# Kernel tuning notes

Hardware: AMD Instinct MI355X
Metric: run time of the kernel (lower is better)

Reference implementation:

```python
import jax, jax.numpy as jnp
import numpy as np

LOG_SCALE_INIT = float(np.log(10.0))


def lorentz_linear(x, W, b, log_scale):
    # nonlin (gelu) -> linear -> Lorentz time/space renormalization
    y = jax.nn.gelu(x) @ W.T + b
    time = jax.nn.sigmoid(y[..., :1]) * jnp.exp(log_scale) + 1.1
    nar = y[..., 1:]
    denom = jnp.clip(jnp.sum(nar * nar, axis=-1, keepdims=True), 1e-8, None)
    scale = (time * time - 1.0) / denom
    return jnp.concatenate([time, nar * jnp.sqrt(scale)], axis=-1)


def ffn_lorentz(x, W1, b1, s1, W2, b2, s2):
    return lorentz_linear(lorentz_linear(x, W1, b1, s1), W2, b2, s2) + x


def knn_indices(x, k):
    # x: (B,N,C). KNN on detached features (as in ViG dense_knn_matrix).
    xs = jax.lax.stop_gradient(x)
    sq = jnp.sum(xs * xs, axis=-1)  # (B,N)
    d = sq[:, :, None] + sq[:, None, :] - 2.0 * jnp.einsum('bnc,bmc->bnm', xs, xs)
    _, idx = jax.lax.top_k(-d, k)  # (B,N,k) nearest (includes self)
    return idx


def graph_conv(x, Wg, bg, sg, k):
    # Max-relative graph conv with Lorentz linear. x: (B,N,C)
    idx = knn_indices(x, k)
    xj = jax.vmap(lambda xb, ib: xb[ib])(x, idx)  # (B,N,k,C) gather
    msg = jnp.max(xj - x[:, :, None, :], axis=2)  # (B,N,C)
    h = jnp.concatenate([x, msg], axis=-1)        # (B,N,2C)
    return lorentz_linear(h, Wg, bg, sg)


def setup_inputs() -> dict:
    key = jax.random.key(0)
    ks = jax.random.split(key, 8)
    B, C, H, W = 8, 192, 56, 56
    x = jax.random.normal(ks[0], (B, C, H, W), dtype=jnp.float32)
    def lin(k_, fin, fout):
        return jax.random.normal(k_, (fout, fin), dtype=jnp.float32) * 0.02
    p = {
        'x': x,
        'W1': lin(ks[1], C, C), 'b1': jnp.zeros((C,), jnp.float32), 's1': jnp.float32(LOG_SCALE_INIT),
        'W2': lin(ks[2], C, C), 'b2': jnp.zeros((C,), jnp.float32), 's2': jnp.float32(LOG_SCALE_INIT),
        'Wg': lin(ks[3], 2 * C, C), 'bg': jnp.zeros((C,), jnp.float32), 'sg': jnp.float32(LOG_SCALE_INIT),
        'W3': lin(ks[4], C, C), 'b3': jnp.zeros((C,), jnp.float32), 's3': jnp.float32(LOG_SCALE_INIT),
        'W4': lin(ks[5], C, C), 'b4': jnp.zeros((C,), jnp.float32), 's4': jnp.float32(LOG_SCALE_INIT),
        'k': 9,
    }
    return p


def reference(x, W1, b1, s1, W2, b2, s2, Wg, bg, sg, W3, b3, s3, W4, b4, s4, k):
    B, C, H, W = x.shape
    xn = x.reshape(B, C, H * W).transpose(0, 2, 1)  # (B,N,C) == rearrange b c (h w) 1 -> b (h w) c
    shortcut = xn
    xn = ffn_lorentz(xn, W1, b1, s1, W2, b2, s2)
    xn = graph_conv(xn, Wg, bg, sg, k)
    xn = ffn_lorentz(xn, W3, b3, s3, W4, b4, s4)
    xn = xn + shortcut  # drop_path = 0 -> identity
    return xn.transpose(0, 2, 1).reshape(B, C, H, W)
```

## Files before the change

kernel.cpp:

```cpp
#include <hip/hip_runtime.h>
#include <math.h>

#define NB   8
#define NC   192
#define NPIX 3136
#define NPAD 3200
#define GRID_LL (NB*98)
#define NIT  25
#define NSP  8
#define GRID_KNN (NB*NIT*NSP)
#define GRID_MSG (NB*196)
#define FINF 3.4e38f

typedef _Float16 f16x8 __attribute__((ext_vector_type(8)));
typedef float   f32x16 __attribute__((ext_vector_type(16)));

__device__ __forceinline__ float gelu_f(float x){
    float u = 0.7978845608028654f * (x + 0.044715f * x * x * x);
    return 0.5f * x * (1.0f + tanhf(u));
}

#define LESS9(da,ia,db,ib) ((da) < (db) || ((da) == (db) && (ia) < (ib)))
#define CSW9(a,ia,b,ib) { bool sw_ = LESS9(b,ib,a,ia); float tf_=(a); int ti_=(ia); \
    (a) = sw_? (b) : (a); (ia) = sw_? (ib) : (ia); (b) = sw_? tf_ : (b); (ib) = sw_? ti_ : (ib); }

struct Top9 {
    float d0,d1,d2,d3,d4,d5,d6,d7,d8;
    int   j0,j1,j2,j3,j4,j5,j6,j7,j8;
    __device__ __forceinline__ void init(){
        d0=d1=d2=d3=d4=d5=d6=d7=d8=FINF;
        j0=j1=j2=j3=j4=j5=j6=j7=j8=0x7FFFFFFF;
    }
    __device__ __forceinline__ void insert(float nd, int ni){
        if (!LESS9(nd, ni, d8, j8)) return;
        d8 = nd; j8 = ni;
        CSW9(d7,j7,d8,j8); CSW9(d6,j6,d7,j7); CSW9(d5,j5,d6,j6); CSW9(d4,j4,d5,j5);
        CSW9(d3,j3,d4,j4); CSW9(d2,j2,d3,j3); CSW9(d1,j1,d2,j2); CSW9(d0,j0,d1,j1);
    }
};

__device__ __forceinline__ unsigned f2mono(float e){
    unsigned u = __float_as_uint(e);
    return u ^ ((unsigned)((int)u >> 31) | 0x80000000u);
}

#define CSK(a,b) { unsigned h_ = (a) > (b) ? (a) : (b); unsigned l_ = (a) > (b) ? (b) : (a); (a) = h_; (b) = l_; }
#define INSKEY(x_) if ((x_) > t_k11){ t_k11 = (x_); \
    CSK(t_k10,t_k11) CSK(t_k9,t_k10) CSK(t_k8,t_k9) CSK(t_k7,t_k8) \
    CSK(t_k6,t_k7) CSK(t_k5,t_k6) CSK(t_k4,t_k5) CSK(t_k3,t_k4) \
    CSK(t_k2,t_k3) CSK(t_k1,t_k2) CSK(t_k0,t_k1) }

#define KQ(A,Q) { \
    unsigned q0_ = (f2mono(A[4*(Q)+0]) & 0xFFFFF000u) | (unsigned)(jinvb_ - 8*(Q)    ); \
    unsigned q1_ = (f2mono(A[4*(Q)+1]) & 0xFFFFF000u) | (unsigned)(jinvb_ - 8*(Q) - 1); \
    unsigned q2_ = (f2mono(A[4*(Q)+2]) & 0xFFFFF000u) | (unsigned)(jinvb_ - 8*(Q) - 2); \
    unsigned q3_ = (f2mono(A[4*(Q)+3]) & 0xFFFFF000u) | (unsigned)(jinvb_ - 8*(Q) - 3); \
    unsigned qa_ = q0_ > q1_ ? q0_ : q1_; \
    unsigned qb_ = q2_ > q3_ ? q2_ : q3_; \
    unsigned qm_ = qa_ > qb_ ? qa_ : qb_; \
    if (qm_ > t_k11){ INSKEY(q0_) INSKEY(q1_) INSKEY(q2_) INSKEY(q3_) } }

#define INSACCK(A,JS) { int jinvb_ = 4095 - (jg + (JS)*32 + 4*h); \
    KQ(A,0) KQ(A,1) KQ(A,2) KQ(A,3) }

#define MF(ACC,AO,BO) ACC = __builtin_amdgcn_mfma_f32_32x32x16_f16(AO,BO,ACC,0,0,0);
#define ZERO16 {0,0,0,0,0,0,0,0,0,0,0,0,0,0,0,0}

__global__ __launch_bounds__(256) void wt_kernel(
    const float* __restrict__ W1, const float* __restrict__ W2,
    const float* __restrict__ Wg, const float* __restrict__ W3,
    const float* __restrict__ W4,
    float* __restrict__ W1T, float* __restrict__ W2T, float* __restrict__ WgT,
    float* __restrict__ W3T, float* __restrict__ W4T)
{
    __shared__ float tile[32*33];
    int t = blockIdx.x;
    const float* src; float* dst; int Kin;
    if (t < 36)      { src = W1; dst = W1T; Kin = 192; }
    else if (t < 72) { src = W2; dst = W2T; Kin = 192; t -= 36; }
    else if (t < 144){ src = Wg; dst = WgT; Kin = 384; t -= 72; }
    else if (t < 180){ src = W3; dst = W3T; Kin = 192; t -= 144; }
    else             { src = W4; dst = W4T; Kin = 192; t -= 180; }
    int ntc = Kin >> 5;
    int tr = t / ntc, tc = t - tr*ntc;
    int tid = threadIdx.x;
    {
        int i = tid >> 3, j4 = (tid & 7)*4;
        float4 v = *(const float4*)&src[(size_t)(tr*32 + i)*Kin + tc*32 + j4];
        tile[i*33 + j4+0] = v.x; tile[i*33 + j4+1] = v.y;
        tile[i*33 + j4+2] = v.z; tile[i*33 + j4+3] = v.w;
    }
    __syncthreads();
    {
        int j = tid >> 3, i4 = (tid & 7)*4;
        float4 o = make_float4(tile[(i4+0)*33 + j], tile[(i4+1)*33 + j],
                               tile[(i4+2)*33 + j], tile[(i4+3)*33 + j]);
        *(float4*)&dst[(size_t)(tc*32 + j)*192 + tr*32 + i4] = o;
    }
}

template<int K, bool DUAL, bool AX, bool AR>
__global__ __launch_bounds__(256, 4) void ll2_kernel(
    const float* __restrict__ A0, const float* __restrict__ A1,
    const float* __restrict__ WT, const float* __restrict__ bias,
    const float* __restrict__ sptr, const float* __restrict__ Xres,
    const float* __restrict__ Rcm,
    float* __restrict__ OutCM, float* __restrict__ Hrm)
{
    __shared__ float lA[32*36];
    __shared__ float lW[32*196];

    const int tid = threadIdx.x;
    const int tx = tid & 15, ty = tid >> 4;
    const int bid = blockIdx.x;
    const int b  = bid / 98;
    const int n0 = (bid % 98) * 32;

    float acc[2][12];
    #pragma unroll
    for (int mi = 0; mi < 2; ++mi)
        #pragma unroll
        for (int j = 0; j < 12; ++j) acc[mi][j] = 0.f;

    for (int kt = 0; kt < K/32; ++kt){
        {
            int kk = tid >> 3;
            int m4 = (tid & 7) * 4;
            int c  = kt*32 + kk;
            const float* pl;
            if (K > 192 && c >= 192) pl = A1 + ((size_t)b*192 + (c - 192))*NPIX;
            else                     pl = A0 + ((size_t)b*192 + c)*NPIX;
            float4 v = *(const float4*)&pl[n0 + m4];
            v.x = gelu_f(v.x); v.y = gelu_f(v.y); v.z = gelu_f(v.z); v.w = gelu_f(v.w);
            *(float4*)&lA[kk*36 + m4] = v;
        }
        #pragma unroll
        for (int r = 0; r < 6; ++r){
            int e  = tid + r*256;
            int kk = e / 48;
            int c4 = (e - kk*48) * 4;
            float4 v = *(const float4*)&WT[(size_t)(kt*32 + kk)*192 + c4];
            *(float4*)&lW[kk*196 + c4] = v;
        }
        __syncthreads();
        #pragma unroll
        for (int kk = 0; kk < 32; ++kk){
            float2 a2 = *(const float2*)&lA[kk*36 + ty*2];
            float4 w0 = *(const float4*)&lW[kk*196 + tx*12];
            float4 w1 = *(const float4*)&lW[kk*196 + tx*12 + 4];
            float4 w2 = *(const float4*)&lW[kk*196 + tx*12 + 8];
            float aw[2]  = {a2.x, a2.y};
            float wv[12] = {w0.x,w0.y,w0.z,w0.w, w1.x,w1.y,w1.z,w1.w, w2.x,w2.y,w2.z,w2.w};
            #pragma unroll
            for (int mi = 0; mi < 2; ++mi)
                #pragma unroll
                for (int j = 0; j < 12; ++j)
                    acc[mi][j] = fmaf(aw[mi], wv[j], acc[mi][j]);
        }
        __syncthreads();
    }

    const int lane = tid & 63;
    float es = expf(sptr[0]);
    float bv[12];
    #pragma unroll
    for (int q = 0; q < 3; ++q){
        float4 t4 = *(const float4*)&bias[tx*12 + q*4];
        bv[q*4+0] = t4.x; bv[q*4+1] = t4.y; bv[q*4+2] = t4.z; bv[q*4+3] = t4.w;
    }
    #pragma unroll
    for (int mi = 0; mi < 2; ++mi){
        float part = 0.f;
        #pragma unroll
        for (int j = 0; j < 12; ++j){
            float y = acc[mi][j] + bv[j];
            acc[mi][j] = y;
            if (!(tx == 0 && j == 0)) part += y * y;
        }
        #pragma unroll
        for (int m = 1; m < 16; m <<= 1) part += __shfl_xor(part, m, 64);
        float y0   = __shfl(acc[mi][0], lane & 48, 64);
        float tval = es / (1.f + expf(-y0)) + 1.1f;
        float denom = fmaxf(part, 1e-8f);
        float sca  = (tval*tval - 1.f) / denom;
        float sqs  = sqrtf(sca);
        #pragma unroll
        for (int j = 0; j < 12; ++j){
            float o = acc[mi][j] * sqs;
            if (tx == 0 && j == 0) o = tval;
            acc[mi][j] = o;
        }
    }
    if (AX){
        #pragma unroll
        for (int j = 0; j < 12; ++j){
            int c = tx*12 + j;
            float2 xv = *(const float2*)&Xres[((size_t)b*192 + c)*NPIX + n0 + ty*2];
            acc[0][j] += xv.x; acc[1][j] += xv.y;
        }
    }
    if (AR){
        #pragma unroll
        for (int j = 0; j < 12; ++j){
            int c = tx*12 + j;
            float2 rv = *(const float2*)&Rcm[((size_t)b*192 + c)*NPIX + n0 + ty*2];
            acc[0][j] += rv.x; acc[1][j] += rv.y;
        }
    }
    #pragma unroll
    for (int j = 0; j < 12; ++j){
        int c = tx*12 + j;
        *(float2*)&OutCM[((size_t)b*192 + c)*NPIX + n0 + ty*2] = make_float2(acc[0][j], acc[1][j]);
    }
    if (DUAL){
        #pragma unroll
        for (int mi = 0; mi < 2; ++mi){
            #pragma unroll
            for (int q = 0; q < 3; ++q){
                float4 o = make_float4(acc[mi][q*4+0], acc[mi][q*4+1], acc[mi][q*4+2], acc[mi][q*4+3]);
                *(float4*)&Hrm[((size_t)b*NPIX + n0 + ty*2 + mi)*192 + tx*12 + q*4] = o;
            }
        }
    }
}

__device__ __forceinline__ unsigned pack2(float a, float b, unsigned &lo){
    union { _Float16 f; unsigned short u; } ha, hb, la, lb;
    ha.f = (_Float16)a; hb.f = (_Float16)b;
    float ra = a - (float)ha.f, rb = b - (float)hb.f;
    la.f = (_Float16)ra; lb.f = (_Float16)rb;
    lo = (unsigned)la.u | ((unsigned)lb.u << 16);
    return (unsigned)ha.u | ((unsigned)hb.u << 16);
}

__global__ __launch_bounds__(256) void conv_kernel(
    const float* __restrict__ H, unsigned short* __restrict__ Xh,
    unsigned short* __restrict__ Xl, unsigned* __restrict__ S2,
    float* __restrict__ SQf)
{
    const int tid = threadIdx.x;
    const int r = blockIdx.x*64 + (tid >> 2);
    const int b = r / NPAD, rl = r - b*NPAD;
    const int part = tid & 3;
    const size_t ob = ((size_t)b*NPAD + rl)*192 + part*48;

    if (rl < NPIX){
        const float* src = H + ((size_t)b*NPIX + rl)*192 + part*48;
        float s = 0.f;
        #pragma unroll
        for (int q = 0; q < 6; ++q){
            float4 v0 = *(const float4*)&src[q*8];
            float4 v1 = *(const float4*)&src[q*8 + 4];
            s = fmaf(v0.x,v0.x, fmaf(v0.y,v0.y, fmaf(v0.z,v0.z, fmaf(v0.w,v0.w, s))));
            s = fmaf(v1.x,v1.x, fmaf(v1.y,v1.y, fmaf(v1.z,v1.z, fmaf(v1.w,v1.w, s))));
            uint4 hv, lv;
            hv.x = pack2(v0.x, v0.y, lv.x);
            hv.y = pack2(v0.z, v0.w, lv.y);
            hv.z = pack2(v1.x, v1.y, lv.z);
            hv.w = pack2(v1.z, v1.w, lv.w);
            *(uint4*)&Xh[ob + q*8] = hv;
            *(uint4*)&Xl[ob + q*8] = lv;
        }
        s += __shfl_xor(s, 1, 64);
        s += __shfl_xor(s, 2, 64);
        if (part == 0){
            SQf[(size_t)b*NPIX + rl] = s;
            float s2 = -0.5f * s;
            union { _Float16 f; unsigned short u; } hh, ll;
            hh.f = (_Float16)s2;
            float rr = s2 - (float)hh.f;
            ll.f = (_Float16)rr;
            S2[(size_t)b*NPAD + rl] = (unsigned)hh.u | ((unsigned)ll.u << 16);
        }
    } else {
        uint4 z = make_uint4(0,0,0,0);
        #pragma unroll
        for (int q = 0; q < 6; ++q){
            *(uint4*)&Xh[ob + q*8] = z;
            *(uint4*)&Xl[ob + q*8] = z;
        }
        if (part == 0){
            union { _Float16 f; unsigned short u; } p;
            p.f = (_Float16)(-30000.0f);
            S2[(size_t)b*NPAD + rl] = (unsigned)p.u;
        }
    }
}

__global__ __launch_bounds__(256) __attribute__((amdgpu_waves_per_eu(2))) void knn_kernel(
    const unsigned short* __restrict__ Xh, const unsigned short* __restrict__ Xl,
    const unsigned* __restrict__ S2, unsigned* __restrict__ PK)
{
    __shared__ uint4 lds[2560];

    const int tid  = threadIdx.x;
    const int lane = tid & 63;
    const int w    = tid >> 6;
    const int l31  = lane & 31;
    const int h    = lane >> 5;
    const int bid  = blockIdx.x;
    const int b    = bid & 7;
    const int t2   = bid >> 3;
    const int itile = t2 >> 3;
    const int sp    = t2 & 7;
    const int i0    = itile * 128;
    const int g0 = (sp*25)/8, g1 = ((sp+1)*25)/8;
    const size_t rowb = (size_t)b * NPAD;

    unsigned t_k0=0,t_k1=0,t_k2=0,t_k3=0,t_k4=0,t_k5=0,
             t_k6=0,t_k7=0,t_k8=0,t_k9=0,t_k10=0,t_k11=0;

    for (int g = g0; g < g1; ++g){
        const int jg = g*128;
        f32x16 acc0 = ZERO16, acc1 = ZERO16, acc2 = ZERO16, acc3 = ZERO16;

        for (int kc = 0; kc < 6; ++kc){
            __syncthreads();
            #pragma unroll
            for (int rr = 0; rr < 8; ++rr){
                int u   = tid + rr*256;
                int arr = u >> 9;
                int rs  = (u >> 2) & 127;
                int seg = u & 3;
                int row = (arr < 2) ? (jg + rs) : (i0 + rs);
                const unsigned short* sptr = (arr & 1) ? Xl : Xh;
                uint4 v = *(const uint4*)&sptr[(rowb + row)*192 + kc*32 + seg*8];
                lds[arr*640 + rs*5 + seg] = v;
            }
            __syncthreads();
            #pragma unroll
            for (int ks = 0; ks < 2; ++ks){
                int kq  = ks*2 + h;
                int rb  = l31*5 + kq;
                f16x8 bh = __builtin_bit_cast(f16x8, lds[1280 + w*160 + rb]);
                f16x8 bl = __builtin_bit_cast(f16x8, lds[1920 + w*160 + rb]);
                f16x8 a0h = __builtin_bit_cast(f16x8, lds[      0 + rb]);
                f16x8 a0l = __builtin_bit_cast(f16x8, lds[640 +   0 + rb]);
                MF(acc0, a0h, bh) MF(acc0, a0l, bh) MF(acc0, a0h, bl)
                f16x8 a1h = __builtin_bit_cast(f16x8, lds[      160 + rb]);
                f16x8 a1l = __builtin_bit_cast(f16x8, lds[640 + 160 + rb]);
                MF(acc1, a1h, bh) MF(acc1, a1l, bh) MF(acc1, a1h, bl)
                f16x8 a2h = __builtin_bit_cast(f16x8, lds[      320 + rb]);
                f16x8 a2l = __builtin_bit_cast(f16x8, lds[640 + 320 + rb]);
                MF(acc2, a2h, bh) MF(acc2, a2l, bh) MF(acc2, a2h, bl)
                f16x8 a3h = __builtin_bit_cast(f16x8, lds[      480 + rb]);
                f16x8 a3l = __builtin_bit_cast(f16x8, lds[640 + 480 + rb]);
                MF(acc3, a3h, bh) MF(acc3, a3l, bh) MF(acc3, a3h, bl)
            }
        }

        {
            unsigned m  = (h == 0) ? 0xFFFFFFFFu : 0u;
            unsigned om = 0x3C00u & m;
            f16x8 one = __builtin_bit_cast(f16x8, make_uint4(om, 0, 0, 0));
            unsigned s0 = S2[rowb + jg +  0 + l31];
            unsigned s1 = S2[rowb + jg + 32 + l31];
            unsigned s2 = S2[rowb + jg + 64 + l31];
            unsigned s3 = S2[rowb + jg + 96 + l31];
            f16x8 a;
            a = __builtin_bit_cast(f16x8, make_uint4((s0 & 0xFFFFu) & m, 0,0,0)); MF(acc0, a, one)
            a = __builtin_bit_cast(f16x8, make_uint4((s0 >> 16)     & m, 0,0,0)); MF(acc0, a, one)
            a = __builtin_bit_cast(f16x8, make_uint4((s1 & 0xFFFFu) & m, 0,0,0)); MF(acc1, a, one)
            a = __builtin_bit_cast(f16x8, make_uint4((s1 >> 16)     & m, 0,0,0)); MF(acc1, a, one)
            a = __builtin_bit_cast(f16x8, make_uint4((s2 & 0xFFFFu) & m, 0,0,0)); MF(acc2, a, one)
            a = __builtin_bit_cast(f16x8, make_uint4((s2 >> 16)     & m, 0,0,0)); MF(acc2, a, one)
            a = __builtin_bit_cast(f16x8, make_uint4((s3 & 0xFFFFu) & m, 0,0,0)); MF(acc3, a, one)
            a = __builtin_bit_cast(f16x8, make_uint4((s3 >> 16)     & m, 0,0,0)); MF(acc3, a, one)
        }

        INSACCK(acc0, 0)
        INSACCK(acc1, 1)
        INSACCK(acc2, 2)
        INSACCK(acc3, 3)
    }

    #define MRGK(Kk) { unsigned ok_ = __shfl((int)(Kk), lane ^ 32, 64); \
                      if (lane < 32) { INSKEY((unsigned)ok_) } }
    MRGK(t_k0) MRGK(t_k1) MRGK(t_k2) MRGK(t_k3) MRGK(t_k4) MRGK(t_k5)
    MRGK(t_k6) MRGK(t_k7) MRGK(t_k8) MRGK(t_k9) MRGK(t_k10) MRGK(t_k11)

    if (lane < 32){
        size_t po = ((size_t)(t2*8 + b)*128 + (size_t)w*32 + l31)*12;
        PK[po+ 0] = t_k0;  PK[po+ 1] = t_k1;  PK[po+ 2] = t_k2;  PK[po+ 3] = t_k3;
        PK[po+ 4] = t_k4;  PK[po+ 5] = t_k5;  PK[po+ 6] = t_k6;  PK[po+ 7] = t_k7;
        PK[po+ 8] = t_k8;  PK[po+ 9] = t_k9;  PK[po+10] = t_k10; PK[po+11] = t_k11;
    }
}

__global__ __launch_bounds__(256) void merge_msg_kernel(
    const float* __restrict__ H, const float* __restrict__ SQf,
    const unsigned* __restrict__ PK, float* __restrict__ Msg)
{
    __shared__ float liX[16*196];
    __shared__ unsigned kv[1600];
    __shared__ float cd[192];
    __shared__ int   cidx[192];
    __shared__ int   fidx[144];

    const int tid = threadIdx.x;
    const int bid = blockIdx.x;
    const int b  = bid / 196;
    const int i0 = (bid % 196) * 16;
    const int base = b * NPIX;

    #pragma unroll
    for (int k = 0; k < 3; ++k){
        int f = tid + k*256;
        int r = f / 48, c4 = f % 48;
        *(float4*)&liX[r*196 + c4*4] = *(const float4*)&H[(size_t)(base + i0 + r)*192 + c4*4];
    }
    if (tid < 128){
        int r = tid >> 3, sp = tid & 7;
        int i = i0 + r;
        size_t po = ((size_t)(((i>>7)*8 + sp)*8 + b)*128 + (i & 127))*12;
        #pragma unroll
        for (int q = 0; q < 3; ++q)
            *(uint4*)&kv[r*100 + sp*12 + q*4] = *(const uint4*)&PK[po + q*4];
    }
    __syncthreads();

    if (tid < 16){
        int r = tid;
        int h0=0,h1=0,h2=0,h3=0,h4=0,h5=0,h6=0,h7=0;
        #pragma unroll
        for (int p = 0; p < 12; ++p){
            unsigned bk = 0; int bs = 0;
#define HEADC(SP,HV) { \
            unsigned k_ = (HV < 12) ? kv[r*100 + SP*12 + HV] : 0u; \
            bool bt_ = k_ > bk; \
            bk = bt_? k_ : bk; bs = bt_? SP : bs; }
            HEADC(0,h0) HEADC(1,h1) HEADC(2,h2) HEADC(3,h3)
            HEADC(4,h4) HEADC(5,h5) HEADC(6,h6) HEADC(7,h7)
#undef HEADC
            cidx[r*12 + p] = 4095 - (int)(bk & 0xFFFu);
            h0 += (bs==0); h1 += (bs==1); h2 += (bs==2); h3 += (bs==3);
            h4 += (bs==4); h5 += (bs==5); h6 += (bs==6); h7 += (bs==7);
        }
    }
    __syncthreads();

    if (tid < 192){
        int r = tid / 12, p = tid - r*12;
        int j = cidx[r*12 + p];
        const float* hj = &H[(size_t)(base + j)*192];
        float dot = 0.f;
        #pragma unroll
        for (int q = 0; q < 48; ++q){
            float4 xv = *(const float4*)&liX[r*196 + q*4];
            float4 yv = *(const float4*)&hj[q*4];
            dot = fmaf(xv.x,yv.x, fmaf(xv.y,yv.y, fmaf(xv.z,yv.z, fmaf(xv.w,yv.w, dot))));
        }
        cd[r*12 + p] = SQf[base + j] - 2.f*dot;
    }
    __syncthreads();

    if (tid < 16){
        int r = tid;
        Top9 m; m.init();
        #pragma unroll
        for (int c = 0; c < 12; ++c) m.insert(cd[r*12 + c], cidx[r*12 + c]);
        fidx[r*9+0]=m.j0; fidx[r*9+1]=m.j1; fidx[r*9+2]=m.j2; fidx[r*9+3]=m.j3;
        fidx[r*9+4]=m.j4; fidx[r*9+5]=m.j5; fidx[r*9+6]=m.j6; fidx[r*9+7]=m.j7;
        fidx[r*9+8]=m.j8;
    }
    __syncthreads();

    int rr = tid & 15, part = tid >> 4;
    int ii = i0 + rr;
    int nbr[9];
    #pragma unroll
    for (int e = 0; e < 9; ++e) nbr[e] = fidx[rr*9 + e];
    #pragma unroll
    for (int q = 0; q < 3; ++q){
        float4 mv = make_float4(-FINF, -FINF, -FINF, -FINF);
        #pragma unroll
        for (int e = 0; e < 9; ++e){
            float4 v = *(const float4*)&H[(size_t)(base + nbr[e])*192 + part*12 + q*4];
            mv.x = fmaxf(mv.x, v.x); mv.y = fmaxf(mv.y, v.y);
            mv.z = fmaxf(mv.z, v.z); mv.w = fmaxf(mv.w, v.w);
        }
        float4 xi = *(const float4*)&liX[rr*196 + part*12 + q*4];
        float m0 = mv.x - xi.x, m1 = mv.y - xi.y, m2 = mv.z - xi.z, m3 = mv.w - xi.w;
        int c = part*12 + q*4;
        Msg[((size_t)b*192 + c+0)*NPIX + ii] = m0;
        Msg[((size_t)b*192 + c+1)*NPIX + ii] = m1;
        Msg[((size_t)b*192 + c+2)*NPIX + ii] = m2;
        Msg[((size_t)b*192 + c+3)*NPIX + ii] = m3;
    }
}

extern "C" void kernel_launch(void* const* d_in, const int* in_sizes, int n_in,
                              void* d_out, int out_size, void* d_ws, size_t ws_size,
                              hipStream_t stream)
{
    const float* x  = (const float*)d_in[0];
    const float* W1 = (const float*)d_in[1];
    const float* b1 = (const float*)d_in[2];
    const float* s1 = (const float*)d_in[3];
    const float* W2 = (const float*)d_in[4];
    const float* b2 = (const float*)d_in[5];
    const float* s2 = (const float*)d_in[6];
    const float* Wg = (const float*)d_in[7];
    const float* bg = (const float*)d_in[8];
    const float* sg = (const float*)d_in[9];
    const float* W3 = (const float*)d_in[10];
    const float* b3 = (const float*)d_in[11];
    const float* s3 = (const float*)d_in[12];
    const float* W4 = (const float*)d_in[13];
    const float* b4 = (const float*)d_in[14];
    const float* s4 = (const float*)d_in[15];

    const size_t PL = (size_t)25088*192;
    float* Hrm  = (float*)d_ws;
    float* X1cm = Hrm  + PL;
    float* T1cm = X1cm + PL;
    float* X2cm = T1cm + PL;
    float* MXr  = X2cm + PL;
    unsigned short* Xh = (unsigned short*)MXr;
    unsigned short* Xl = Xh + (size_t)NB*NPAD*192;
    float* Msg = MXr;
    unsigned* S2p = (unsigned*)(MXr + (size_t)NB*NPAD*192/2*2);
    float* SQf = (float*)(S2p + (size_t)NB*NPAD);
    float* W1T = SQf + (size_t)NB*NPIX;
    float* W2T = W1T + 36864;
    float* WgT = W2T + 36864;
    float* W3T = WgT + 73728;
    float* W4T = W3T + 36864;
    unsigned* PK = (unsigned*)X2cm;
    float* out = (float*)d_out;

    wt_kernel<<<216, 256, 0, stream>>>(W1, W2, Wg, W3, W4, W1T, W2T, WgT, W3T, W4T);
    ll2_kernel<192, false, false, false><<<GRID_LL, 256, 0, stream>>>(x,    x,    W1T, b1, s1, nullptr, nullptr, T1cm, nullptr);
    ll2_kernel<192, true , true , false><<<GRID_LL, 256, 0, stream>>>(T1cm, T1cm, W2T, b2, s2, x,       nullptr, X1cm, Hrm);
    conv_kernel<<<NB*NPAD/64, 256, 0, stream>>>(Hrm, Xh, Xl, S2p, SQf);
    knn_kernel<<<GRID_KNN, 256, 0, stream>>>(Xh, Xl, S2p, PK);
    merge_msg_kernel<<<GRID_MSG, 256, 0, stream>>>(Hrm, SQf, PK, Msg);
    ll2_kernel<384, false, false, false><<<GRID_LL, 256, 0, stream>>>(X1cm, Msg,  WgT, bg, sg, nullptr, nullptr, X2cm, nullptr);
    ll2_kernel<192, false, false, false><<<GRID_LL, 256, 0, stream>>>(X2cm, X2cm, W3T, b3, s3, nullptr, nullptr, T1cm, nullptr);
    ll2_kernel<192, false, true , true ><<<GRID_LL, 256, 0, stream>>>(T1cm, T1cm, W4T, b4, s4, x,       X2cm,    out,  nullptr);
}
```

Before: 527.0 us.

## Halve LL tile rows, cut KNN splits to 4, add float threshold early-out

The Lorentz-linear kernel now handles 16 pixels per block instead of 32, which doubles the grid but also doubles the number of times the weight tile is loaded per output. The KNN kernel splits the candidate range into 4 parts instead of 8, so each block scans more columns and the merge step reads fewer partial lists. Each 16-value accumulator now gets a float max check against the current 12th-best key before any key packing or insertion, which skips insert work once the candidate list has filled. The smaller KNN grid may reduce parallelism, and the LL change raises weight traffic per output.

```diff
diff --git a/kernel.cpp b/kernel.cpp
--- a/kernel.cpp
+++ b/kernel.cpp
@@ -5,9 +5,9 @@
 #define NC   192
 #define NPIX 3136
 #define NPAD 3200
-#define GRID_LL (NB*98)
+#define GRID_LL (NB*196)
 #define NIT  25
-#define NSP  8
+#define NSP  4
 #define GRID_KNN (NB*NIT*NSP)
 #define GRID_MSG (NB*196)
 #define FINF 3.4e38f
@@ -42,6 +42,9 @@
 __device__ __forceinline__ unsigned f2mono(float e){
     unsigned u = __float_as_uint(e);
     return u ^ ((unsigned)((int)u >> 31) | 0x80000000u);
+}
+__device__ __forceinline__ float unmono(unsigned m){
+    return __uint_as_float(m ^ ((unsigned)(((int)~m) >> 31) | 0x80000000u));
 }
 
 #define CSK(a,b) { unsigned h_ = (a) > (b) ? (a) : (b); unsigned l_ = (a) > (b) ? (b) : (a); (a) = h_; (b) = l_; }
@@ -60,8 +63,12 @@
     unsigned qm_ = qa_ > qb_ ? qa_ : qb_; \
     if (qm_ > t_k11){ INSKEY(q0_) INSKEY(q1_) INSKEY(q2_) INSKEY(q3_) } }
 
-#define INSACCK(A,JS) { int jinvb_ = 4095 - (jg + (JS)*32 + 4*h); \
-    KQ(A,0) KQ(A,1) KQ(A,2) KQ(A,3) }
+#define AMAX16(A) fmaxf(fmaxf(fmaxf(fmaxf(A[0],A[1]),fmaxf(A[2],A[3])),fmaxf(fmaxf(A[4],A[5]),fmaxf(A[6],A[7]))), \
+                        fmaxf(fmaxf(fmaxf(A[8],A[9]),fmaxf(A[10],A[11])),fmaxf(fmaxf(A[12],A[13]),fmaxf(A[14],A[15]))))
+
+#define INSACCK(A,JS) { float am_ = AMAX16(A); \
+    if (am_ >= thrf){ int jinvb_ = 4095 - (jg + (JS)*32 + 4*h); \
+        KQ(A,0) KQ(A,1) KQ(A,2) KQ(A,3) } }
 
 #define MF(ACC,AO,BO) ACC = __builtin_amdgcn_mfma_f32_32x32x16_f16(AO,BO,ACC,0,0,0);
 #define ZERO16 {0,0,0,0,0,0,0,0,0,0,0,0,0,0,0,0}
@@ -107,32 +114,30 @@
     const float* __restrict__ Rcm,
     float* __restrict__ OutCM, float* __restrict__ Hrm)
 {
-    __shared__ float lA[32*36];
+    __shared__ float lA[32*20];
     __shared__ float lW[32*196];
 
     const int tid = threadIdx.x;
     const int tx = tid & 15, ty = tid >> 4;
     const int bid = blockIdx.x;
-    const int b  = bid / 98;
-    const int n0 = (bid % 98) * 32;
-
-    float acc[2][12];
+    const int b  = bid / 196;
+    const int n0 = (bid % 196) * 16;
+
+    float acc[12];
     #pragma unroll
-    for (int mi = 0; mi < 2; ++mi)
-        #pragma unroll
-        for (int j = 0; j < 12; ++j) acc[mi][j] = 0.f;
+    for (int j = 0; j < 12; ++j) acc[j] = 0.f;
 
     for (int kt = 0; kt < K/32; ++kt){
-        {
-            int kk = tid >> 3;
-            int m4 = (tid & 7) * 4;
+        if (tid < 128){
+            int kk = tid >> 2;
+            int m4 = (tid & 3) * 4;
             int c  = kt*32 + kk;
             const float* pl;
             if (K > 192 && c >= 192) pl = A1 + ((size_t)b*192 + (c - 192))*NPIX;
             else                     pl = A0 + ((size_t)b*192 + c)*NPIX;
             float4 v = *(const float4*)&pl[n0 + m4];
             v.x = gelu_f(v.x); v.y = gelu_f(v.y); v.z = gelu_f(v.z); v.w = gelu_f(v.w);
-            *(float4*)&lA[kk*36 + m4] = v;
+            *(float4*)&lA[kk*20 + m4] = v;
         }
         #pragma unroll
         for (int r = 0; r < 6; ++r){
@@ -145,17 +150,14 @@
         __syncthreads();
         #pragma unroll
         for (int kk = 0; kk < 32; ++kk){
-            float2 a2 = *(const float2*)&lA[kk*36 + ty*2];
+            float a  = lA[kk*20 + ty];
             float4 w0 = *(const float4*)&lW[kk*196 + tx*12];
             float4 w1 = *(const float4*)&lW[kk*196 + tx*12 + 4];
             float4 w2 = *(const float4*)&lW[kk*196 + tx*12 + 8];
-            float aw[2]  = {a2.x, a2.y};
             float wv[12] = {w0.x,w0.y,w0.z,w0.w, w1.x,w1.y,w1.z,w1.w, w2.x,w2.y,w2.z,w2.w};
             #pragma unroll
-            for (int mi = 0; mi < 2; ++mi)
-                #pragma unroll
-                for (int j = 0; j < 12; ++j)
-                    acc[mi][j] = fmaf(aw[mi], wv[j], acc[mi][j]);
+            for (int j = 0; j < 12; ++j)
+                acc[j] = fmaf(a, wv[j], acc[j]);
         }
         __syncthreads();
     }
@@ -168,58 +170,52 @@
         float4 t4 = *(const float4*)&bias[tx*12 + q*4];
         bv[q*4+0] = t4.x; bv[q*4+1] = t4.y; bv[q*4+2] = t4.z; bv[q*4+3] = t4.w;
     }
-    #pragma unroll
-    for (int mi = 0; mi < 2; ++mi){
+    {
         float part = 0.f;
         #pragma unroll
         for (int j = 0; j < 12; ++j){
-            float y = acc[mi][j] + bv[j];
-            acc[mi][j] = y;
+            float y = acc[j] + bv[j];
+            acc[j] = y;
             if (!(tx == 0 && j == 0)) part += y * y;
         }
         #pragma unroll
         for (int m = 1; m < 16; m <<= 1) part += __shfl_xor(part, m, 64);
-        float y0   = __shfl(acc[mi][0], lane & 48, 64);
+        float y0   = __shfl(acc[0], lane & 48, 64);
         float tval = es / (1.f + expf(-y0)) + 1.1f;
         float denom = fmaxf(part, 1e-8f);
         float sca  = (tval*tval - 1.f) / denom;
         float sqs  = sqrtf(sca);
         #pragma unroll
         for (int j = 0; j < 12; ++j){
-            float o = acc[mi][j] * sqs;
+            float o = acc[j] * sqs;
             if (tx == 0 && j == 0) o = tval;
-            acc[mi][j] = o;
+            acc[j] = o;
         }
     }
     if (AX){
         #pragma unroll
         for (int j = 0; j < 12; ++j){
             int c = tx*12 + j;
-            float2 xv = *(const float2*)&Xres[((size_t)b*192 + c)*NPIX + n0 + ty*2];
-            acc[0][j] += xv.x; acc[1][j] += xv.y;
+            acc[j] += Xres[((size_t)b*192 + c)*NPIX + n0 + ty];
         }
     }
     if (AR){
         #pragma unroll
         for (int j = 0; j < 12; ++j){
             int c = tx*12 + j;
-            float2 rv = *(const float2*)&Rcm[((size_t)b*192 + c)*NPIX + n0 + ty*2];
-            acc[0][j] += rv.x; acc[1][j] += rv.y;
+            acc[j] += Rcm[((size_t)b*192 + c)*NPIX + n0 + ty];
         }
     }
     #pragma unroll
     for (int j = 0; j < 12; ++j){
         int c = tx*12 + j;
-        *(float2*)&OutCM[((size_t)b*192 + c)*NPIX + n0 + ty*2] = make_float2(acc[0][j], acc[1][j]);
+        OutCM[((size_t)b*192 + c)*NPIX + n0 + ty] = acc[j];
     }
     if (DUAL){
         #pragma unroll
-        for (int mi = 0; mi < 2; ++mi){
-            #pragma unroll
-            for (int q = 0; q < 3; ++q){
-                float4 o = make_float4(acc[mi][q*4+0], acc[mi][q*4+1], acc[mi][q*4+2], acc[mi][q*4+3]);
-                *(float4*)&Hrm[((size_t)b*NPIX + n0 + ty*2 + mi)*192 + tx*12 + q*4] = o;
-            }
+        for (int q = 0; q < 3; ++q){
+            float4 o = make_float4(acc[q*4+0], acc[q*4+1], acc[q*4+2], acc[q*4+3]);
+            *(float4*)&Hrm[((size_t)b*NPIX + n0 + ty)*192 + tx*12 + q*4] = o;
         }
     }
 }
@@ -301,14 +297,15 @@
     const int bid  = blockIdx.x;
     const int b    = bid & 7;
     const int t2   = bid >> 3;
-    const int itile = t2 >> 3;
-    const int sp    = t2 & 7;
+    const int itile = t2 >> 2;
+    const int sp    = t2 & 3;
     const int i0    = itile * 128;
-    const int g0 = (sp*25)/8, g1 = ((sp+1)*25)/8;
+    const int g0 = (sp*25)/NSP, g1 = ((sp+1)*25)/NSP;
     const size_t rowb = (size_t)b * NPAD;
 
     unsigned t_k0=0,t_k1=0,t_k2=0,t_k3=0,t_k4=0,t_k5=0,
              t_k6=0,t_k7=0,t_k8=0,t_k9=0,t_k10=0,t_k11=0;
+    float thrf = -FINF;
 
     for (int g = g0; g < g1; ++g){
         const int jg = g*128;
@@ -372,6 +369,7 @@
         INSACCK(acc1, 1)
         INSACCK(acc2, 2)
         INSACCK(acc3, 3)
+        thrf = (t_k11 != 0u) ? unmono(t_k11 & 0xFFFFF000u) : -FINF;
     }
 
     #define MRGK(Kk) { unsigned ok_ = __shfl((int)(Kk), lane ^ 32, 64); \
@@ -392,7 +390,7 @@
     const unsigned* __restrict__ PK, float* __restrict__ Msg)
 {
     __shared__ float liX[16*196];
-    __shared__ unsigned kv[1600];
+    __shared__ unsigned kv[16*52];
     __shared__ float cd[192];
     __shared__ int   cidx[192];
     __shared__ int   fidx[144];
@@ -409,32 +407,30 @@
         int r = f / 48, c4 = f % 48;
         *(float4*)&liX[r*196 + c4*4] = *(const float4*)&H[(size_t)(base + i0 + r)*192 + c4*4];
     }
-    if (tid < 128){
-        int r = tid >> 3, sp = tid & 7;
+    if (tid < 64){
+        int r = tid >> 2, sp = tid & 3;
         int i = i0 + r;
-        size_t po = ((size_t)(((i>>7)*8 + sp)*8 + b)*128 + (i & 127))*12;
+        size_t po = ((size_t)(((i>>7)*NSP + sp)*8 + b)*128 + (i & 127))*12;
         #pragma unroll
         for (int q = 0; q < 3; ++q)
-            *(uint4*)&kv[r*100 + sp*12 + q*4] = *(const uint4*)&PK[po + q*4];
+            *(uint4*)&kv[r*52 + sp*12 + q*4] = *(const uint4*)&PK[po + q*4];
     }
     __syncthreads();
 
     if (tid < 16){
         int r = tid;
-        int h0=0,h1=0,h2=0,h3=0,h4=0,h5=0,h6=0,h7=0;
+        int h0=0,h1=0,h2=0,h3=0;
         #pragma unroll
         for (int p = 0; p < 12; ++p){
             unsigned bk = 0; int bs = 0;
 #define HEADC(SP,HV) { \
-            unsigned k_ = (HV < 12) ? kv[r*100 + SP*12 + HV] : 0u; \
+            unsigned k_ = (HV < 12) ? kv[r*52 + SP*12 + HV] : 0u; \
             bool bt_ = k_ > bk; \
             bk = bt_? k_ : bk; bs = bt_? SP : bs; }
             HEADC(0,h0) HEADC(1,h1) HEADC(2,h2) HEADC(3,h3)
-            HEADC(4,h4) HEADC(5,h5) HEADC(6,h6) HEADC(7,h7)
 #undef HEADC
             cidx[r*12 + p] = 4095 - (int)(bk & 0xFFFu);
             h0 += (bs==0); h1 += (bs==1); h2 += (bs==2); h3 += (bs==3);
-            h4 += (bs==4); h5 += (bs==5); h6 += (bs==6); h7 += (bs==7);
         }
     }
     __syncthreads();
```

Result: slower. 639.9 us (+21.4%).
